# Kernel tuning notes

Hardware: AMD Instinct MI355X
Metric: run time of the kernel (lower is better)

Reference implementation:

```python
import jax, jax.numpy as jnp
import numpy as np

NUM_EMBEDDINGS = 1024
EMBEDDING_DIM = 64

def setup_inputs() -> dict:
    key = jax.random.key(0)
    k1, k2 = jax.random.split(key)
    x = jax.random.normal(k1, (16, 64, 64, EMBEDDING_DIM), dtype=jnp.float32)
    # tf.random_uniform_initializer default: U(-0.05, 0.05)
    embeddings = jax.random.uniform(k2, (EMBEDDING_DIM, NUM_EMBEDDINGS),
                                    dtype=jnp.float32, minval=-0.05, maxval=0.05)
    return {"x": x, "embeddings": embeddings}

def reference(x, embeddings):
    input_shape = x.shape
    D = embeddings.shape[0]
    flat = x.reshape(-1, D)  # [N, D]
    # squared L2 distances: ||z||^2 + ||e||^2 - 2 z.e
    similarity = flat @ embeddings  # [N, K]
    distances = (jnp.sum(flat * flat, axis=1, keepdims=True)
                 + jnp.sum(embeddings * embeddings, axis=0)
                 - 2.0 * similarity)
    indices = jnp.argmin(distances, axis=1)  # [N]
    # one-hot @ embeddings.T == gather rows of embeddings.T
    quantized = jnp.take(embeddings.T, indices, axis=0)  # [N, D]
    return quantized.reshape(input_shape)
```

## Files before the change

### kernel.cpp

```cpp
#include <hip/hip_runtime.h>
#include <float.h>

#define K_CODES 1024
#define DIM 64
#define BR 128
#define SAFE_MARGIN_H 1.25e-4f

typedef __attribute__((ext_vector_type(8))) short bf16x8;
typedef __attribute__((ext_vector_type(8))) unsigned short u16x8;
typedef __attribute__((ext_vector_type(4))) float f32x4;

__device__ __forceinline__ unsigned short f2bf(float f) {
    unsigned int u = __float_as_uint(f);
    u += 0x7fff + ((u >> 16) & 1);
    return (unsigned short)(u >> 16);
}
__device__ __forceinline__ float bf2f(unsigned short h) {
    return __uint_as_float(((unsigned int)h) << 16);
}
__device__ __forceinline__ int swz(int row, int byteInRow) {
    return row * 128 + (byteInRow ^ ((row & 7) << 4));
}

__global__ __launch_bounds__(256) void vq_prep2(
    const float* __restrict__ E, float* __restrict__ Et,
    unsigned short* __restrict__ Eh, unsigned short* __restrict__ El,
    float* __restrict__ nrm, float* __restrict__ nrm2)
{
    __shared__ float T[64 * 17];
    const int t = threadIdx.x;
    const int k0 = blockIdx.x * 16;
    #pragma unroll
    for (int i = 0; i < 4; ++i) {
        int idx = i * 256 + t;
        int d = idx >> 4, kk = idx & 15;
        T[d * 17 + kk] = E[d * K_CODES + k0 + kk];
    }
    __syncthreads();
    #pragma unroll
    for (int i = 0; i < 4; ++i) {
        int idx = i * 256 + t;
        int kk = idx >> 6, d = idx & 63;
        float v = T[d * 17 + kk];
        Et[(size_t)(k0 + kk) * DIM + d] = v;
        unsigned short h = f2bf(v);
        Eh[(size_t)(k0 + kk) * DIM + d] = h;
        El[(size_t)(k0 + kk) * DIM + d] = f2bf(v - bf2f(h));
    }
    if (t < 16) {
        float s = 0.f;
        #pragma unroll
        for (int d = 0; d < DIM; ++d) {
            float v = T[d * 17 + t];
            s = __builtin_fmaf(v, v, s);
        }
        nrm [k0 + t] = s;
        nrm2[k0 + t] = 0.5f * s;
    }
}

__global__ __launch_bounds__(256, 2) void vq_mfma(
    const float* __restrict__ x,
    const float* __restrict__ E,
    const unsigned short* __restrict__ Eh,
    const unsigned short* __restrict__ El,
    const float* __restrict__ nrm,
    const float* __restrict__ nrm2,
    const float* __restrict__ Et,
    float* __restrict__ out)
{
    __shared__ char lds[32768 + 512 + 512 + 16];
    char* Ah = lds;
    char* Al = lds + 16384;
    char* Bh = lds;
    char* Bl = lds + 16384;
    int*  bidx  = (int*)(lds + 32768);
    int*  flist = (int*)(lds + 33280);
    int*  fcnt  = (int*)(lds + 33792);

    const int t    = threadIdx.x;
    const int lane = t & 63;
    const int wv   = t >> 6;
    const int col  = lane & 15;
    const int q    = lane >> 4;
    const int koff = q * 16;
    const long r0  = (long)blockIdx.x * BR;

    if (t == 0) *fcnt = 0;

    {
        int row = t >> 1, h = t & 1;
        const float4* src = (const float4*)(x + (r0 + row) * DIM + h * 32);
        float v[32];
        #pragma unroll
        for (int i = 0; i < 8; ++i) {
            float4 f = src[i];
            v[4*i+0] = -f.x; v[4*i+1] = -f.y; v[4*i+2] = -f.z; v[4*i+3] = -f.w;
        }
        unsigned short hi[32], lo[32];
        #pragma unroll
        for (int i = 0; i < 32; ++i) {
            hi[i] = f2bf(v[i]);
            lo[i] = f2bf(v[i] - bf2f(hi[i]));
        }
        #pragma unroll
        for (int s = 0; s < 2; ++s) {
            int seg = h * 2 + s;
            *(u16x8*)(Ah + swz(row, seg*32))      = *(u16x8*)(hi + s*16);
            *(u16x8*)(Ah + swz(row, seg*32 + 16)) = *(u16x8*)(hi + s*16 + 8);
            *(u16x8*)(Al + swz(row, seg*32))      = *(u16x8*)(lo + s*16);
            *(u16x8*)(Al + swz(row, seg*32 + 16)) = *(u16x8*)(lo + s*16 + 8);
        }
    }
    __syncthreads();

    bf16x8 aH[2][2], aL[2][2];
    #pragma unroll
    for (int m = 0; m < 2; ++m) {
        int arow = wv * 32 + m * 16 + col;
        #pragma unroll
        for (int kk = 0; kk < 2; ++kk) {
            aH[m][kk] = *(bf16x8*)(Ah + swz(arow, kk*64 + koff));
            aL[m][kk] = *(bf16x8*)(Al + swz(arow, kk*64 + koff));
        }
    }
    __syncthreads();

    float b1[2][4], b2[2][4];
    int   i1[2][4];
    #pragma unroll
    for (int m = 0; m < 2; ++m)
        #pragma unroll
        for (int j = 0; j < 4; ++j) { b1[m][j] = FLT_MAX; b2[m][j] = FLT_MAX; i1[m][j] = 0x7fffffff; }

    for (int c0 = 0; c0 < K_CODES; c0 += 128) {
        #pragma unroll
        for (int i = 0; i < 4; ++i) {
            int idx = i * 256 + t;
            int cr = idx >> 3, sg = idx & 7;
            *(u16x8*)(Bh + swz(cr, sg*16)) = *(const u16x8*)(Eh + (size_t)(c0+cr)*DIM + sg*8);
            *(u16x8*)(Bl + swz(cr, sg*16)) = *(const u16x8*)(El + (size_t)(c0+cr)*DIM + sg*8);
        }
        __syncthreads();

        #pragma unroll
        for (int nt = 0; nt < 8; ++nt) {
            int brow = nt * 16 + col;
            bf16x8 bH0 = *(bf16x8*)(Bh + swz(brow, koff));
            bf16x8 bH1 = *(bf16x8*)(Bh + swz(brow, 64 + koff));
            bf16x8 bL0 = *(bf16x8*)(Bl + swz(brow, koff));
            bf16x8 bL1 = *(bf16x8*)(Bl + swz(brow, 64 + koff));
            int code = c0 + nt * 16 + col;
            float ne2 = nrm2[code];
            #pragma unroll
            for (int m = 0; m < 2; ++m) {
                f32x4 acc = {ne2, ne2, ne2, ne2};
                acc = __builtin_amdgcn_mfma_f32_16x16x32_bf16(aH[m][0], bH0, acc, 0,0,0);
                acc = __builtin_amdgcn_mfma_f32_16x16x32_bf16(aH[m][1], bH1, acc, 0,0,0);
                acc = __builtin_amdgcn_mfma_f32_16x16x32_bf16(aH[m][0], bL0, acc, 0,0,0);
                acc = __builtin_amdgcn_mfma_f32_16x16x32_bf16(aH[m][1], bL1, acc, 0,0,0);
                acc = __builtin_amdgcn_mfma_f32_16x16x32_bf16(aL[m][0], bH0, acc, 0,0,0);
                acc = __builtin_amdgcn_mfma_f32_16x16x32_bf16(aL[m][1], bH1, acc, 0,0,0);
                #pragma unroll
                for (int j = 0; j < 4; ++j) {
                    float d = acc[j];
                    bool lt = d < b1[m][j];
                    float nb1 = fminf(b1[m][j], d);
                    b2[m][j] = __builtin_amdgcn_fmed3f(b1[m][j], b2[m][j], d);
                    i1[m][j] = lt ? code : i1[m][j];
                    b1[m][j] = nb1;
                }
            }
        }
        __syncthreads();
    }

    #pragma unroll
    for (int msk = 1; msk < 16; msk <<= 1) {
        #pragma unroll
        for (int m = 0; m < 2; ++m)
            #pragma unroll
            for (int j = 0; j < 4; ++j) {
                float o1 = __shfl_xor(b1[m][j], msk, 64);
                int   oi = __shfl_xor(i1[m][j], msk, 64);
                float o2 = __shfl_xor(b2[m][j], msk, 64);
                bool take = (o1 < b1[m][j]) || (o1 == b1[m][j] && oi < i1[m][j]);
                float worst = take ? b1[m][j] : o1;
                if (take) { b1[m][j] = o1; i1[m][j] = oi; }
                b2[m][j] = fminf(fminf(b2[m][j], o2), worst);
            }
    }
    if (col == 0) {
        #pragma unroll
        for (int m = 0; m < 2; ++m)
            #pragma unroll
            for (int j = 0; j < 4; ++j) {
                int rowl = wv * 32 + m * 16 + q * 4 + j;
                bidx[rowl] = i1[m][j];
                if (b2[m][j] - b1[m][j] <= SAFE_MARGIN_H) {
                    int p = atomicAdd(fcnt, 1);
                    flist[p] = rowl;
                }
            }
    }
    __syncthreads();

    {
        int rowl = t >> 1, h = t & 1;
        int code = bidx[rowl];
        const float4* src = (const float4*)(Et + (size_t)code * DIM + h * 32);
        float4* dst = (float4*)(out + (size_t)(r0 + rowl) * DIM + h * 32);
        #pragma unroll
        for (int i = 0; i < 8; ++i) dst[i] = src[i];
    }
    __syncthreads();

    const int nf = *fcnt;
    if (nf > 0) {
        float* zsh    = (float*)lds;
        float* rv     = (float*)(lds + 1024);
        int*   ri     = (int*)  (lds + 1088);
        int*   winner = (int*)  (lds + 1152);
        for (int f = 0; f < nf; ++f) {
            int rowl = flist[f];
            if (t < DIM) zsh[t] = x[(r0 + rowl) * DIM + t];
            __syncthreads();
            float zn = 0.f;
            #pragma unroll
            for (int d = 0; d < DIM; ++d) zn = __builtin_fmaf(zsh[d], zsh[d], zn);
            float a0 = 0.f, a1 = 0.f, a2 = 0.f, a3 = 0.f;
            #pragma unroll
            for (int d = 0; d < DIM; ++d) {
                float zd = zsh[d];
                const float* Ed = E + d * K_CODES;
                a0 = __builtin_fmaf(zd, Ed[t      ], a0);
                a1 = __builtin_fmaf(zd, Ed[t + 256], a1);
                a2 = __builtin_fmaf(zd, Ed[t + 512], a2);
                a3 = __builtin_fmaf(zd, Ed[t + 768], a3);
            }
            float d0 = __builtin_fmaf(-2.f, a0, zn + nrm[t      ]);
            float d1 = __builtin_fmaf(-2.f, a1, zn + nrm[t + 256]);
            float d2 = __builtin_fmaf(-2.f, a2, zn + nrm[t + 512]);
            float d3 = __builtin_fmaf(-2.f, a3, zn + nrm[t + 768]);
            float bv = d0; int bi = t;
            if (d1 < bv) { bv = d1; bi = t + 256; }
            if (d2 < bv) { bv = d2; bi = t + 512; }
            if (d3 < bv) { bv = d3; bi = t + 768; }
            #pragma unroll
            for (int m = 1; m < 64; m <<= 1) {
                float ov = __shfl_xor(bv, m, 64);
                int   oi = __shfl_xor(bi, m, 64);
                if (ov < bv || (ov == bv && oi < bi)) { bv = ov; bi = oi; }
            }
            if (lane == 0) { rv[wv] = bv; ri[wv] = bi; }
            __syncthreads();
            if (t == 0) {
                float v = rv[0]; int b = ri[0];
                #pragma unroll
                for (int w = 1; w < 4; ++w)
                    if (rv[w] < v || (rv[w] == v && ri[w] < b)) { v = rv[w]; b = ri[w]; }
                *winner = b;
            }
            __syncthreads();
            if (t < DIM) out[(r0 + rowl) * DIM + t] = Et[(size_t)(*winner) * DIM + t];
            __syncthreads();
        }
    }
}

extern "C" void kernel_launch(void* const* d_in, const int* in_sizes, int n_in,
                              void* d_out, int out_size, void* d_ws, size_t ws_size,
                              hipStream_t stream) {
    const float* x = (const float*)d_in[0];
    const float* E = (const float*)d_in[1];
    float* out = (float*)d_out;

    char* ws = (char*)d_ws;
    float*          Et   = (float*)ws;
    unsigned short* Eh   = (unsigned short*)(ws + 262144);
    unsigned short* El   = (unsigned short*)(ws + 393216);
    float*          nrm  = (float*)(ws + 524288);
    float*          nrm2 = (float*)(ws + 528384);

    int nrows = in_sizes[0] / DIM;

    vq_prep2<<<64, 256, 0, stream>>>(E, Et, Eh, El, nrm, nrm2);
    vq_mfma<<<nrows / BR, 256, 0, stream>>>(x, E, Eh, El, nrm, nrm2, Et, out);
}
```

Baseline: 123.5 us.

## Halve rows per block and move near-tie refinement into a separate global kernel

Each block now handles 64 rows instead of 128, which doubles the grid to 1024 blocks and halves the per-wave A fragment and register state. Ambiguous rows are no longer refined serially inside the block that found them. They are appended to a global list through an atomic counter and handled by a new 512-block refine kernel. The refine tail should then no longer stall individual blocks, and parallelism improves. The cost is an extra kernel launch, and every block now reloads the codebook tiles, doubling codebook traffic from L2.

Result: no change. 121.5 us (-1.6%).

```diff
diff --git a/kernel.cpp b/kernel.cpp
--- a/kernel.cpp
+++ b/kernel.cpp
@@ -3,7 +3,7 @@
 
 #define K_CODES 1024
 #define DIM 64
-#define BR 128
+#define BR 64
 #define SAFE_MARGIN_H 1.25e-4f
 
 typedef __attribute__((ext_vector_type(8))) short bf16x8;
@@ -25,11 +25,12 @@
 __global__ __launch_bounds__(256) void vq_prep2(
     const float* __restrict__ E, float* __restrict__ Et,
     unsigned short* __restrict__ Eh, unsigned short* __restrict__ El,
-    float* __restrict__ nrm, float* __restrict__ nrm2)
+    float* __restrict__ nrm, float* __restrict__ nrm2, int* __restrict__ cnt)
 {
     __shared__ float T[64 * 17];
     const int t = threadIdx.x;
     const int k0 = blockIdx.x * 16;
+    if (blockIdx.x == 0 && t == 0) *cnt = 0;
     #pragma unroll
     for (int i = 0; i < 4; ++i) {
         int idx = i * 256 + t;
@@ -61,22 +62,19 @@
 
 __global__ __launch_bounds__(256, 2) void vq_mfma(
     const float* __restrict__ x,
-    const float* __restrict__ E,
     const unsigned short* __restrict__ Eh,
     const unsigned short* __restrict__ El,
-    const float* __restrict__ nrm,
     const float* __restrict__ nrm2,
     const float* __restrict__ Et,
-    float* __restrict__ out)
+    float* __restrict__ out,
+    int* __restrict__ cnt, int* __restrict__ list)
 {
-    __shared__ char lds[32768 + 512 + 512 + 16];
+    __shared__ char lds[32768 + 256];
     char* Ah = lds;
-    char* Al = lds + 16384;
+    char* Al = lds + 8192;
     char* Bh = lds;
     char* Bl = lds + 16384;
-    int*  bidx  = (int*)(lds + 32768);
-    int*  flist = (int*)(lds + 33280);
-    int*  fcnt  = (int*)(lds + 33792);
+    int*  bidx = (int*)(lds + 32768);
 
     const int t    = threadIdx.x;
     const int lane = t & 63;
@@ -86,52 +84,43 @@
     const int koff = q * 16;
     const long r0  = (long)blockIdx.x * BR;
 
-    if (t == 0) *fcnt = 0;
-
     {
-        int row = t >> 1, h = t & 1;
-        const float4* src = (const float4*)(x + (r0 + row) * DIM + h * 32);
-        float v[32];
-        #pragma unroll
-        for (int i = 0; i < 8; ++i) {
+        int row = t >> 2, qh = t & 3;
+        const float4* src = (const float4*)(x + (r0 + row) * DIM + qh * 16);
+        float v[16];
+        #pragma unroll
+        for (int i = 0; i < 4; ++i) {
             float4 f = src[i];
             v[4*i+0] = -f.x; v[4*i+1] = -f.y; v[4*i+2] = -f.z; v[4*i+3] = -f.w;
         }
-        unsigned short hi[32], lo[32];
-        #pragma unroll
-        for (int i = 0; i < 32; ++i) {
+        unsigned short hi[16], lo[16];
+        #pragma unroll
+        for (int i = 0; i < 16; ++i) {
             hi[i] = f2bf(v[i]);
             lo[i] = f2bf(v[i] - bf2f(hi[i]));
         }
-        #pragma unroll
-        for (int s = 0; s < 2; ++s) {
-            int seg = h * 2 + s;
-            *(u16x8*)(Ah + swz(row, seg*32))      = *(u16x8*)(hi + s*16);
-            *(u16x8*)(Ah + swz(row, seg*32 + 16)) = *(u16x8*)(hi + s*16 + 8);
-            *(u16x8*)(Al + swz(row, seg*32))      = *(u16x8*)(lo + s*16);
-            *(u16x8*)(Al + swz(row, seg*32 + 16)) = *(u16x8*)(lo + s*16 + 8);
-        }
-    }
-    __syncthreads();
-
-    bf16x8 aH[2][2], aL[2][2];
-    #pragma unroll
-    for (int m = 0; m < 2; ++m) {
-        int arow = wv * 32 + m * 16 + col;
+        *(u16x8*)(Ah + swz(row, qh*32))      = *(u16x8*)(hi);
+        *(u16x8*)(Ah + swz(row, qh*32 + 16)) = *(u16x8*)(hi + 8);
+        *(u16x8*)(Al + swz(row, qh*32))      = *(u16x8*)(lo);
+        *(u16x8*)(Al + swz(row, qh*32 + 16)) = *(u16x8*)(lo + 8);
+    }
+    __syncthreads();
+
+    bf16x8 aH[2], aL[2];
+    {
+        int arow = wv * 16 + col;
         #pragma unroll
         for (int kk = 0; kk < 2; ++kk) {
-            aH[m][kk] = *(bf16x8*)(Ah + swz(arow, kk*64 + koff));
-            aL[m][kk] = *(bf16x8*)(Al + swz(arow, kk*64 + koff));
-        }
-    }
-    __syncthreads();
-
-    float b1[2][4], b2[2][4];
-    int   i1[2][4];
-    #pragma unroll
-    for (int m = 0; m < 2; ++m)
-        #pragma unroll
-        for (int j = 0; j < 4; ++j) { b1[m][j] = FLT_MAX; b2[m][j] = FLT_MAX; i1[m][j] = 0x7fffffff; }
+            aH[kk] = *(bf16x8*)(Ah + swz(arow, kk*64 + koff));
+            aL[kk] = *(bf16x8*)(Al + swz(arow, kk*64 + koff));
+        }
+    }
+    __syncthreads();
+
+    float b1[4], b2[4];
+    int   i1[4];
+    #pragma unroll
+    for (int j = 0; j < 4; ++j) { b1[j] = FLT_MAX; b2[j] = FLT_MAX; i1[j] = 0x7fffffff; }
 
     for (int c0 = 0; c0 < K_CODES; c0 += 128) {
         #pragma unroll
@@ -152,119 +141,119 @@
             bf16x8 bL1 = *(bf16x8*)(Bl + swz(brow, 64 + koff));
             int code = c0 + nt * 16 + col;
             float ne2 = nrm2[code];
-            #pragma unroll
-            for (int m = 0; m < 2; ++m) {
-                f32x4 acc = {ne2, ne2, ne2, ne2};
-                acc = __builtin_amdgcn_mfma_f32_16x16x32_bf16(aH[m][0], bH0, acc, 0,0,0);
-                acc = __builtin_amdgcn_mfma_f32_16x16x32_bf16(aH[m][1], bH1, acc, 0,0,0);
-                acc = __builtin_amdgcn_mfma_f32_16x16x32_bf16(aH[m][0], bL0, acc, 0,0,0);
-                acc = __builtin_amdgcn_mfma_f32_16x16x32_bf16(aH[m][1], bL1, acc, 0,0,0);
-                acc = __builtin_amdgcn_mfma_f32_16x16x32_bf16(aL[m][0], bH0, acc, 0,0,0);
-                acc = __builtin_amdgcn_mfma_f32_16x16x32_bf16(aL[m][1], bH1, acc, 0,0,0);
-                #pragma unroll
-                for (int j = 0; j < 4; ++j) {
-                    float d = acc[j];
-                    bool lt = d < b1[m][j];
-                    float nb1 = fminf(b1[m][j], d);
-                    b2[m][j] = __builtin_amdgcn_fmed3f(b1[m][j], b2[m][j], d);
-                    i1[m][j] = lt ? code : i1[m][j];
-                    b1[m][j] = nb1;
-                }
-            }
-        }
-        __syncthreads();
-    }
-
-    #pragma unroll
-    for (int msk = 1; msk < 16; msk <<= 1) {
-        #pragma unroll
-        for (int m = 0; m < 2; ++m)
+            f32x4 acc = {ne2, ne2, ne2, ne2};
+            acc = __builtin_amdgcn_mfma_f32_16x16x32_bf16(aH[0], bH0, acc, 0,0,0);
+            acc = __builtin_amdgcn_mfma_f32_16x16x32_bf16(aH[1], bH1, acc, 0,0,0);
+            acc = __builtin_amdgcn_mfma_f32_16x16x32_bf16(aH[0], bL0, acc, 0,0,0);
+            acc = __builtin_amdgcn_mfma_f32_16x16x32_bf16(aH[1], bL1, acc, 0,0,0);
+            acc = __builtin_amdgcn_mfma_f32_16x16x32_bf16(aL[0], bH0, acc, 0,0,0);
+            acc = __builtin_amdgcn_mfma_f32_16x16x32_bf16(aL[1], bH1, acc, 0,0,0);
             #pragma unroll
             for (int j = 0; j < 4; ++j) {
-                float o1 = __shfl_xor(b1[m][j], msk, 64);
-                int   oi = __shfl_xor(i1[m][j], msk, 64);
-                float o2 = __shfl_xor(b2[m][j], msk, 64);
-                bool take = (o1 < b1[m][j]) || (o1 == b1[m][j] && oi < i1[m][j]);
-                float worst = take ? b1[m][j] : o1;
-                if (take) { b1[m][j] = o1; i1[m][j] = oi; }
-                b2[m][j] = fminf(fminf(b2[m][j], o2), worst);
+                float d = acc[j];
+                bool lt = d < b1[j];
+                float nb1 = fminf(b1[j], d);
+                b2[j] = __builtin_amdgcn_fmed3f(b1[j], b2[j], d);
+                i1[j] = lt ? code : i1[j];
+                b1[j] = nb1;
             }
+        }
+        __syncthreads();
+    }
+
+    #pragma unroll
+    for (int msk = 1; msk < 16; msk <<= 1) {
+        #pragma unroll
+        for (int j = 0; j < 4; ++j) {
+            float o1 = __shfl_xor(b1[j], msk, 64);
+            int   oi = __shfl_xor(i1[j], msk, 64);
+            float o2 = __shfl_xor(b2[j], msk, 64);
+            bool take = (o1 < b1[j]) || (o1 == b1[j] && oi < i1[j]);
+            float worst = take ? b1[j] : o1;
+            if (take) { b1[j] = o1; i1[j] = oi; }
+            b2[j] = fminf(fminf(b2[j], o2), worst);
+        }
     }
     if (col == 0) {
         #pragma unroll
-        for (int m = 0; m < 2; ++m)
+        for (int j = 0; j < 4; ++j) {
+            int rowl = wv * 16 + q * 4 + j;
+            bidx[rowl] = i1[j];
+            if (b2[j] - b1[j] <= SAFE_MARGIN_H) {
+                int p = atomicAdd(cnt, 1);
+                list[p] = (int)(r0 + rowl);
+            }
+        }
+    }
+    __syncthreads();
+
+    {
+        int row = t >> 2, qh = t & 3;
+        int code = bidx[row];
+        const float4* src = (const float4*)(Et + (size_t)code * DIM + qh * 16);
+        float4* dst = (float4*)(out + (size_t)(r0 + row) * DIM + qh * 16);
+        #pragma unroll
+        for (int i = 0; i < 4; ++i) dst[i] = src[i];
+    }
+}
+
+__global__ __launch_bounds__(256) void vq_refine3(
+    const float* __restrict__ x, const float* __restrict__ E,
+    const float* __restrict__ Et, const float* __restrict__ nrm,
+    float* __restrict__ out,
+    const int* __restrict__ cnt, const int* __restrict__ list)
+{
+    __shared__ float zsh[DIM];
+    __shared__ float rv[4];
+    __shared__ int   ri[4];
+    __shared__ int   winner;
+    const int n = *cnt;
+    const int t = threadIdx.x;
+    const int lane = t & 63, wv = t >> 6;
+
+    for (int i = blockIdx.x; i < n; i += gridDim.x) {
+        int row = list[i];
+        if (t < DIM) zsh[t] = x[(size_t)row * DIM + t];
+        __syncthreads();
+        float zn = 0.f;
+        #pragma unroll
+        for (int d = 0; d < DIM; ++d) zn = __builtin_fmaf(zsh[d], zsh[d], zn);
+        float a0 = 0.f, a1 = 0.f, a2 = 0.f, a3 = 0.f;
+        #pragma unroll
+        for (int d = 0; d < DIM; ++d) {
+            float zd = zsh[d];
+            const float* Ed = E + d * K_CODES;
+            a0 = __builtin_fmaf(zd, Ed[t      ], a0);
+            a1 = __builtin_fmaf(zd, Ed[t + 256], a1);
+            a2 = __builtin_fmaf(zd, Ed[t + 512], a2);
+            a3 = __builtin_fmaf(zd, Ed[t + 768], a3);
+        }
+        float d0 = __builtin_fmaf(-2.f, a0, zn + nrm[t      ]);
+        float d1 = __builtin_fmaf(-2.f, a1, zn + nrm[t + 256]);
+        float d2 = __builtin_fmaf(-2.f, a2, zn + nrm[t + 512]);
+        float d3 = __builtin_fmaf(-2.f, a3, zn + nrm[t + 768]);
+        float bv = d0; int bi = t;
+        if (d1 < bv) { bv = d1; bi = t + 256; }
+        if (d2 < bv) { bv = d2; bi = t + 512; }
+        if (d3 < bv) { bv = d3; bi = t + 768; }
+        #pragma unroll
+        for (int m = 1; m < 64; m <<= 1) {
+            float ov = __shfl_xor(bv, m, 64);
+            int   oi = __shfl_xor(bi, m, 64);
+            if (ov < bv || (ov == bv && oi < bi)) { bv = ov; bi = oi; }
+        }
+        if (lane == 0) { rv[wv] = bv; ri[wv] = bi; }
+        __syncthreads();
+        if (t == 0) {
+            float v = rv[0]; int b = ri[0];
             #pragma unroll
-            for (int j = 0; j < 4; ++j) {
-                int rowl = wv * 32 + m * 16 + q * 4 + j;
-                bidx[rowl] = i1[m][j];
-                if (b2[m][j] - b1[m][j] <= SAFE_MARGIN_H) {
-                    int p = atomicAdd(fcnt, 1);
-                    flist[p] = rowl;
-                }
-            }
-    }
-    __syncthreads();
-
-    {
-        int rowl = t >> 1, h = t & 1;
-        int code = bidx[rowl];
-        const float4* src = (const float4*)(Et + (size_t)code * DIM + h * 32);
-        float4* dst = (float4*)(out + (size_t)(r0 + rowl) * DIM + h * 32);
-        #pragma unroll
-        for (int i = 0; i < 8; ++i) dst[i] = src[i];
-    }
-    __syncthreads();
-
-    const int nf = *fcnt;
-    if (nf > 0) {
-        float* zsh    = (float*)lds;
-        float* rv     = (float*)(lds + 1024);
-        int*   ri     = (int*)  (lds + 1088);
-        int*   winner = (int*)  (lds + 1152);
-        for (int f = 0; f < nf; ++f) {
-            int rowl = flist[f];
-            if (t < DIM) zsh[t] = x[(r0 + rowl) * DIM + t];
-            __syncthreads();
-            float zn = 0.f;
-            #pragma unroll
-            for (int d = 0; d < DIM; ++d) zn = __builtin_fmaf(zsh[d], zsh[d], zn);
-            float a0 = 0.f, a1 = 0.f, a2 = 0.f, a3 = 0.f;
-            #pragma unroll
-            for (int d = 0; d < DIM; ++d) {
-                float zd = zsh[d];
-                const float* Ed = E + d * K_CODES;
-                a0 = __builtin_fmaf(zd, Ed[t      ], a0);
-                a1 = __builtin_fmaf(zd, Ed[t + 256], a1);
-                a2 = __builtin_fmaf(zd, Ed[t + 512], a2);
-                a3 = __builtin_fmaf(zd, Ed[t + 768], a3);
-            }
-            float d0 = __builtin_fmaf(-2.f, a0, zn + nrm[t      ]);
-            float d1 = __builtin_fmaf(-2.f, a1, zn + nrm[t + 256]);
-            float d2 = __builtin_fmaf(-2.f, a2, zn + nrm[t + 512]);
-            float d3 = __builtin_fmaf(-2.f, a3, zn + nrm[t + 768]);
-            float bv = d0; int bi = t;
-            if (d1 < bv) { bv = d1; bi = t + 256; }
-            if (d2 < bv) { bv = d2; bi = t + 512; }
-            if (d3 < bv) { bv = d3; bi = t + 768; }
-            #pragma unroll
-            for (int m = 1; m < 64; m <<= 1) {
-                float ov = __shfl_xor(bv, m, 64);
-                int   oi = __shfl_xor(bi, m, 64);
-                if (ov < bv || (ov == bv && oi < bi)) { bv = ov; bi = oi; }
-            }
-            if (lane == 0) { rv[wv] = bv; ri[wv] = bi; }
-            __syncthreads();
-            if (t == 0) {
-                float v = rv[0]; int b = ri[0];
-                #pragma unroll
-                for (int w = 1; w < 4; ++w)
-                    if (rv[w] < v || (rv[w] == v && ri[w] < b)) { v = rv[w]; b = ri[w]; }
-                *winner = b;
-            }
-            __syncthreads();
-            if (t < DIM) out[(r0 + rowl) * DIM + t] = Et[(size_t)(*winner) * DIM + t];
-            __syncthreads();
-        }
+            for (int w = 1; w < 4; ++w)
+                if (rv[w] < v || (rv[w] == v && ri[w] < b)) { v = rv[w]; b = ri[w]; }
+            winner = b;
+        }
+        __syncthreads();
+        if (t < DIM) out[(size_t)row * DIM + t] = Et[(size_t)winner * DIM + t];
+        __syncthreads();
     }
 }
 
@@ -281,9 +270,12 @@
     unsigned short* El   = (unsigned short*)(ws + 393216);
     float*          nrm  = (float*)(ws + 524288);
     float*          nrm2 = (float*)(ws + 528384);
+    int*            cnt  = (int*)(ws + 532480);
+    int*            list = (int*)(ws + 532736);
 
     int nrows = in_sizes[0] / DIM;
 
-    vq_prep2<<<64, 256, 0, stream>>>(E, Et, Eh, El, nrm, nrm2);
-    vq_mfma<<<nrows / BR, 256, 0, stream>>>(x, E, Eh, El, nrm, nrm2, Et, out);
-}
+    vq_prep2<<<64, 256, 0, stream>>>(E, Et, Eh, El, nrm, nrm2, cnt);
+    vq_mfma<<<nrows / BR, 256, 0, stream>>>(x, Eh, El, nrm2, Et, out, cnt, list);
+    vq_refine3<<<512, 256, 0, stream>>>(x, E, Et, nrm, out, cnt, list);
+}
```

## Stream codebook directly from global with register prefetch and split refinement kernel

Applied to the files above, without the earlier changes.

The main kernel no longer stages codebook tiles through shared memory with block barriers. Each wave now loads bf16 hi/lo codebook fragments straight from global/L2 into registers, using a four-deep software prefetch ring. Ambiguous rows go to a global list instead of being refined serially inside each block, and a separate grid-strided refine kernel processes that list. The aim is to remove barrier stalls and LDS traffic and to stop the serial tail from holding up blocks. The cost is higher register pressure, redundant global loads across waves, and an extra kernel launch.

Measured after the change: 145.8 us. 1.18x slower.

```diff
diff --git a/kernel.cpp b/kernel.cpp
--- a/kernel.cpp
+++ b/kernel.cpp
@@ -25,11 +25,12 @@
 __global__ __launch_bounds__(256) void vq_prep2(
     const float* __restrict__ E, float* __restrict__ Et,
     unsigned short* __restrict__ Eh, unsigned short* __restrict__ El,
-    float* __restrict__ nrm, float* __restrict__ nrm2)
+    float* __restrict__ nrm, float* __restrict__ nrm2, int* __restrict__ cnt)
 {
     __shared__ float T[64 * 17];
     const int t = threadIdx.x;
     const int k0 = blockIdx.x * 16;
+    if (blockIdx.x == 0 && t == 0) *cnt = 0;
     #pragma unroll
     for (int i = 0; i < 4; ++i) {
         int idx = i * 256 + t;
@@ -59,24 +60,53 @@
     }
 }
 
+#define LOADG(BH0, BH1, BL0, BL1, NE, g) do {                              \
+    int _c = (g) * 16 + col;                                               \
+    const unsigned short* _pe = Eh + (size_t)_c * DIM + q * 8;             \
+    const unsigned short* _pl = El + (size_t)_c * DIM + q * 8;             \
+    BH0 = *(const bf16x8*)(_pe);                                           \
+    BH1 = *(const bf16x8*)(_pe + 32);                                      \
+    BL0 = *(const bf16x8*)(_pl);                                           \
+    BL1 = *(const bf16x8*)(_pl + 32);                                      \
+    NE  = nrm2[_c];                                                        \
+} while (0)
+
+#define COMP(BH0, BH1, BL0, BL1, NE, g) do {                               \
+    int _code = (g) * 16 + col;                                            \
+    _Pragma("unroll")                                                      \
+    for (int m = 0; m < 2; ++m) {                                          \
+        f32x4 acc = {NE, NE, NE, NE};       \
+        acc = __builtin_amdgcn_mfma_f32_16x16x32_bf16(aH[m][0], BH0, acc, 0,0,0); \
+        acc = __builtin_amdgcn_mfma_f32_16x16x32_bf16(aH[m][1], BH1, acc, 0,0,0); \
+        acc = __builtin_amdgcn_mfma_f32_16x16x32_bf16(aH[m][0], BL0, acc, 0,0,0); \
+        acc = __builtin_amdgcn_mfma_f32_16x16x32_bf16(aH[m][1], BL1, acc, 0,0,0); \
+        acc = __builtin_amdgcn_mfma_f32_16x16x32_bf16(aL[m][0], BH0, acc, 0,0,0); \
+        acc = __builtin_amdgcn_mfma_f32_16x16x32_bf16(aL[m][1], BH1, acc, 0,0,0); \
+        _Pragma("unroll")                                                  \
+        for (int j = 0; j < 4; ++j) {                                      \
+            float _d = acc[j];                                             \
+            bool _lt = _d < b1[m][j];                                      \
+            float _nb1 = fminf(b1[m][j], _d);                              \
+            b2[m][j] = __builtin_amdgcn_fmed3f(b1[m][j], b2[m][j], _d);    \
+            i1[m][j] = _lt ? _code : i1[m][j];                             \
+            b1[m][j] = _nb1;                                               \
+        }                                                                  \
+    }                                                                      \
+} while (0)
+
 __global__ __launch_bounds__(256, 2) void vq_mfma(
     const float* __restrict__ x,
-    const float* __restrict__ E,
     const unsigned short* __restrict__ Eh,
     const unsigned short* __restrict__ El,
-    const float* __restrict__ nrm,
     const float* __restrict__ nrm2,
     const float* __restrict__ Et,
-    float* __restrict__ out)
+    float* __restrict__ out,
+    int* __restrict__ cnt, int* __restrict__ list)
 {
-    __shared__ char lds[32768 + 512 + 512 + 16];
+    __shared__ char lds[32768 + 512];
     char* Ah = lds;
     char* Al = lds + 16384;
-    char* Bh = lds;
-    char* Bl = lds + 16384;
-    int*  bidx  = (int*)(lds + 32768);
-    int*  flist = (int*)(lds + 33280);
-    int*  fcnt  = (int*)(lds + 33792);
+    int*  bidx = (int*)(lds + 32768);
 
     const int t    = threadIdx.x;
     const int lane = t & 63;
@@ -86,8 +116,6 @@
     const int koff = q * 16;
     const long r0  = (long)blockIdx.x * BR;
 
-    if (t == 0) *fcnt = 0;
-
     {
         int row = t >> 1, h = t & 1;
         const float4* src = (const float4*)(x + (r0 + row) * DIM + h * 32);
@@ -124,7 +152,6 @@
             aL[m][kk] = *(bf16x8*)(Al + swz(arow, kk*64 + koff));
         }
     }
-    __syncthreads();
 
     float b1[2][4], b2[2][4];
     int   i1[2][4];
@@ -133,46 +160,24 @@
         #pragma unroll
         for (int j = 0; j < 4; ++j) { b1[m][j] = FLT_MAX; b2[m][j] = FLT_MAX; i1[m][j] = 0x7fffffff; }
 
-    for (int c0 = 0; c0 < K_CODES; c0 += 128) {
-        #pragma unroll
-        for (int i = 0; i < 4; ++i) {
-            int idx = i * 256 + t;
-            int cr = idx >> 3, sg = idx & 7;
-            *(u16x8*)(Bh + swz(cr, sg*16)) = *(const u16x8*)(Eh + (size_t)(c0+cr)*DIM + sg*8);
-            *(u16x8*)(Bl + swz(cr, sg*16)) = *(const u16x8*)(El + (size_t)(c0+cr)*DIM + sg*8);
-        }
-        __syncthreads();
-
-        #pragma unroll
-        for (int nt = 0; nt < 8; ++nt) {
-            int brow = nt * 16 + col;
-            bf16x8 bH0 = *(bf16x8*)(Bh + swz(brow, koff));
-            bf16x8 bH1 = *(bf16x8*)(Bh + swz(brow, 64 + koff));
-            bf16x8 bL0 = *(bf16x8*)(Bl + swz(brow, koff));
-            bf16x8 bL1 = *(bf16x8*)(Bl + swz(brow, 64 + koff));
-            int code = c0 + nt * 16 + col;
-            float ne2 = nrm2[code];
-            #pragma unroll
-            for (int m = 0; m < 2; ++m) {
-                f32x4 acc = {ne2, ne2, ne2, ne2};
-                acc = __builtin_amdgcn_mfma_f32_16x16x32_bf16(aH[m][0], bH0, acc, 0,0,0);
-                acc = __builtin_amdgcn_mfma_f32_16x16x32_bf16(aH[m][1], bH1, acc, 0,0,0);
-                acc = __builtin_amdgcn_mfma_f32_16x16x32_bf16(aH[m][0], bL0, acc, 0,0,0);
-                acc = __builtin_amdgcn_mfma_f32_16x16x32_bf16(aH[m][1], bL1, acc, 0,0,0);
-                acc = __builtin_amdgcn_mfma_f32_16x16x32_bf16(aL[m][0], bH0, acc, 0,0,0);
-                acc = __builtin_amdgcn_mfma_f32_16x16x32_bf16(aL[m][1], bH1, acc, 0,0,0);
-                #pragma unroll
-                for (int j = 0; j < 4; ++j) {
-                    float d = acc[j];
-                    bool lt = d < b1[m][j];
-                    float nb1 = fminf(b1[m][j], d);
-                    b2[m][j] = __builtin_amdgcn_fmed3f(b1[m][j], b2[m][j], d);
-                    i1[m][j] = lt ? code : i1[m][j];
-                    b1[m][j] = nb1;
-                }
-            }
-        }
-        __syncthreads();
+    bf16x8 p0h0, p0h1, p0l0, p0l1;  float p0n;
+    bf16x8 p1h0, p1h1, p1l0, p1l1;  float p1n;
+    bf16x8 p2h0, p2h1, p2l0, p2l1;  float p2n;
+    bf16x8 p3h0, p3h1, p3l0, p3l1;  float p3n;
+    LOADG(p0h0, p0h1, p0l0, p0l1, p0n, 0);
+    LOADG(p1h0, p1h1, p1l0, p1l1, p1n, 1);
+    LOADG(p2h0, p2h1, p2l0, p2l1, p2n, 2);
+    LOADG(p3h0, p3h1, p3l0, p3l1, p3n, 3);
+    #pragma unroll 1
+    for (int nt = 0; nt < 64; nt += 4) {
+        COMP (p0h0, p0h1, p0l0, p0l1, p0n, nt);
+        LOADG(p0h0, p0h1, p0l0, p0l1, p0n, (nt + 4) & 63);
+        COMP (p1h0, p1h1, p1l0, p1l1, p1n, nt + 1);
+        LOADG(p1h0, p1h1, p1l0, p1l1, p1n, (nt + 5) & 63);
+        COMP (p2h0, p2h1, p2l0, p2l1, p2n, nt + 2);
+        LOADG(p2h0, p2h1, p2l0, p2l1, p2n, (nt + 6) & 63);
+        COMP (p3h0, p3h1, p3l0, p3l1, p3n, nt + 3);
+        LOADG(p3h0, p3h1, p3l0, p3l1, p3n, (nt + 7) & 63);
     }
 
     #pragma unroll
@@ -198,8 +203,8 @@
                 int rowl = wv * 32 + m * 16 + q * 4 + j;
                 bidx[rowl] = i1[m][j];
                 if (b2[m][j] - b1[m][j] <= SAFE_MARGIN_H) {
-                    int p = atomicAdd(fcnt, 1);
-                    flist[p] = rowl;
+                    int p = atomicAdd(cnt, 1);
+                    list[p] = (int)(r0 + rowl);
                 }
             }
     }
@@ -213,58 +218,65 @@
         #pragma unroll
         for (int i = 0; i < 8; ++i) dst[i] = src[i];
     }
-    __syncthreads();
-
-    const int nf = *fcnt;
-    if (nf > 0) {
-        float* zsh    = (float*)lds;
-        float* rv     = (float*)(lds + 1024);
-        int*   ri     = (int*)  (lds + 1088);
-        int*   winner = (int*)  (lds + 1152);
-        for (int f = 0; f < nf; ++f) {
-            int rowl = flist[f];
-            if (t < DIM) zsh[t] = x[(r0 + rowl) * DIM + t];
-            __syncthreads();
-            float zn = 0.f;
+}
+
+__global__ __launch_bounds__(256) void vq_refine3(
+    const float* __restrict__ x, const float* __restrict__ E,
+    const float* __restrict__ Et, const float* __restrict__ nrm,
+    float* __restrict__ out,
+    const int* __restrict__ cnt, const int* __restrict__ list)
+{
+    __shared__ float zsh[DIM];
+    __shared__ float rv[4];
+    __shared__ int   ri[4];
+    __shared__ int   winner;
+    const int n = *cnt;
+    const int t = threadIdx.x;
+    const int lane = t & 63, wv = t >> 6;
+
+    for (int i = blockIdx.x; i < n; i += gridDim.x) {
+        int row = list[i];
+        if (t < DIM) zsh[t] = x[(size_t)row * DIM + t];
+        __syncthreads();
+        float zn = 0.f;
+        #pragma unroll
+        for (int d = 0; d < DIM; ++d) zn = __builtin_fmaf(zsh[d], zsh[d], zn);
+        float a0 = 0.f, a1 = 0.f, a2 = 0.f, a3 = 0.f;
+        #pragma unroll
+        for (int d = 0; d < DIM; ++d) {
+            float zd = zsh[d];
+            const float* Ed = E + d * K_CODES;
+            a0 = __builtin_fmaf(zd, Ed[t      ], a0);
+            a1 = __builtin_fmaf(zd, Ed[t + 256], a1);
+            a2 = __builtin_fmaf(zd, Ed[t + 512], a2);
+            a3 = __builtin_fmaf(zd, Ed[t + 768], a3);
+        }
+        float d0 = __builtin_fmaf(-2.f, a0, zn + nrm[t      ]);
+        float d1 = __builtin_fmaf(-2.f, a1, zn + nrm[t + 256]);
+        float d2 = __builtin_fmaf(-2.f, a2, zn + nrm[t + 512]);
+        float d3 = __builtin_fmaf(-2.f, a3, zn + nrm[t + 768]);
+        float bv = d0; int bi = t;
+        if (d1 < bv) { bv = d1; bi = t + 256; }
+        if (d2 < bv) { bv = d2; bi = t + 512; }
+        if (d3 < bv) { bv = d3; bi = t + 768; }
+        #pragma unroll
+        for (int m = 1; m < 64; m <<= 1) {
+            float ov = __shfl_xor(bv, m, 64);
+            int   oi = __shfl_xor(bi, m, 64);
+            if (ov < bv || (ov == bv && oi < bi)) { bv = ov; bi = oi; }
+        }
+        if (lane == 0) { rv[wv] = bv; ri[wv] = bi; }
+        __syncthreads();
+        if (t == 0) {
+            float v = rv[0]; int b = ri[0];
             #pragma unroll
-            for (int d = 0; d < DIM; ++d) zn = __builtin_fmaf(zsh[d], zsh[d], zn);
-            float a0 = 0.f, a1 = 0.f, a2 = 0.f, a3 = 0.f;
-            #pragma unroll
-            for (int d = 0; d < DIM; ++d) {
-                float zd = zsh[d];
-                const float* Ed = E + d * K_CODES;
-                a0 = __builtin_fmaf(zd, Ed[t      ], a0);
-                a1 = __builtin_fmaf(zd, Ed[t + 256], a1);
-                a2 = __builtin_fmaf(zd, Ed[t + 512], a2);
-                a3 = __builtin_fmaf(zd, Ed[t + 768], a3);
-            }
-            float d0 = __builtin_fmaf(-2.f, a0, zn + nrm[t      ]);
-            float d1 = __builtin_fmaf(-2.f, a1, zn + nrm[t + 256]);
-            float d2 = __builtin_fmaf(-2.f, a2, zn + nrm[t + 512]);
-            float d3 = __builtin_fmaf(-2.f, a3, zn + nrm[t + 768]);
-            float bv = d0; int bi = t;
-            if (d1 < bv) { bv = d1; bi = t + 256; }
-            if (d2 < bv) { bv = d2; bi = t + 512; }
-            if (d3 < bv) { bv = d3; bi = t + 768; }
-            #pragma unroll
-            for (int m = 1; m < 64; m <<= 1) {
-                float ov = __shfl_xor(bv, m, 64);
-                int   oi = __shfl_xor(bi, m, 64);
-                if (ov < bv || (ov == bv && oi < bi)) { bv = ov; bi = oi; }
-            }
-            if (lane == 0) { rv[wv] = bv; ri[wv] = bi; }
-            __syncthreads();
-            if (t == 0) {
-                float v = rv[0]; int b = ri[0];
-                #pragma unroll
-                for (int w = 1; w < 4; ++w)
-                    if (rv[w] < v || (rv[w] == v && ri[w] < b)) { v = rv[w]; b = ri[w]; }
-                *winner = b;
-            }
-            __syncthreads();
-            if (t < DIM) out[(r0 + rowl) * DIM + t] = Et[(size_t)(*winner) * DIM + t];
-            __syncthreads();
-        }
+            for (int w = 1; w < 4; ++w)
+                if (rv[w] < v || (rv[w] == v && ri[w] < b)) { v = rv[w]; b = ri[w]; }
+            winner = b;
+        }
+        __syncthreads();
+        if (t < DIM) out[(size_t)row * DIM + t] = Et[(size_t)winner * DIM + t];
+        __syncthreads();
     }
 }
 
@@ -281,9 +293,12 @@
     unsigned short* El   = (unsigned short*)(ws + 393216);
     float*          nrm  = (float*)(ws + 524288);
     float*          nrm2 = (float*)(ws + 528384);
+    int*            cnt  = (int*)(ws + 532480);
+    int*            list = (int*)(ws + 532736);
 
     int nrows = in_sizes[0] / DIM;
 
-    vq_prep2<<<64, 256, 0, stream>>>(E, Et, Eh, El, nrm, nrm2);
-    vq_mfma<<<nrows / BR, 256, 0, stream>>>(x, E, Eh, El, nrm, nrm2, Et, out);
-}
+    vq_prep2<<<64, 256, 0, stream>>>(E, Et, Eh, El, nrm, nrm2, cnt);
+    vq_mfma<<<nrows / BR, 256, 0, stream>>>(x, Eh, El, nrm2, Et, out, cnt, list);
+    vq_refine3<<<512, 256, 0, stream>>>(x, E, Et, nrm, out, cnt, list);
+}
```
